# Performance work log

Measured on AMD Instinct MI355X. Metric: run time of the kernel, lower is better.

Reference implementation:

```python
import jax, jax.numpy as jnp
import numpy as np
from jax import lax

DIM = 256
NUM_HEADS = 8
AREA = 4
HEAD_DIM = DIM // NUM_HEADS


def setup_inputs() -> dict:
    key = jax.random.key(0)
    ks = jax.random.split(key, 7)
    B, C, H, W = 4, DIM, 64, 64
    x = jax.random.normal(ks[0], (B, C, H, W), dtype=jnp.float32)
    s = 0.02
    w_qkv = jax.random.normal(ks[1], (3 * C, C), dtype=jnp.float32) * s
    b_qkv = jnp.zeros((3 * C,), dtype=jnp.float32)
    w_pe = jax.random.normal(ks[2], (C, 1, 7, 7), dtype=jnp.float32) * s  # depthwise
    b_pe = jnp.zeros((C,), dtype=jnp.float32)
    w_proj = jax.random.normal(ks[3], (C, C), dtype=jnp.float32) * s
    b_proj = jnp.zeros((C,), dtype=jnp.float32)
    return {"x": x, "w_qkv": w_qkv, "b_qkv": b_qkv, "w_pe": w_pe,
            "b_pe": b_pe, "w_proj": w_proj, "b_proj": b_proj}


def _conv1x1(x, w, b):
    # x: [B,C,H,W], w: [O,C] -> [B,O,H,W]
    return jnp.einsum('bchw,oc->bohw', x, w) + b[None, :, None, None]


def _dwconv7(x, w, b):
    # depthwise 7x7, pad 3, groups = C
    y = lax.conv_general_dilated(
        x, w, window_strides=(1, 1), padding=[(3, 3), (3, 3)],
        dimension_numbers=('NCHW', 'OIHW', 'NCHW'),
        feature_group_count=x.shape[1])
    return y + b[None, :, None, None]


def reference(x, w_qkv, b_qkv, w_pe, b_pe, w_proj, b_proj):
    B, C, H, W = x.shape
    N = H * W
    nh, hd, area = NUM_HEADS, HEAD_DIM, AREA
    Na = N // area
    Ba = B * area

    qkv = _conv1x1(x, w_qkv, b_qkv)                    # [B,3C,H,W]
    qkv = qkv.reshape(B, 3 * C, N).transpose(0, 2, 1)  # [B,N,3C]
    qkv = qkv.reshape(Ba, Na, nh, 3, hd)               # split heads / q,k,v
    q = qkv[:, :, :, 0, :]                             # [Ba,Na,nh,hd]
    k = qkv[:, :, :, 1, :]
    v = qkv[:, :, :, 2, :]

    scale = jnp.asarray(hd, x.dtype) ** -0.5
    attn = jnp.einsum('bihd,bjhd->bhij', q, k) * scale  # [Ba,nh,Na,Na]
    attn = jax.nn.softmax(attn, axis=-1)
    out = jnp.einsum('bhij,bjhd->bihd', attn, v)        # [Ba,Na,nh,hd]

    out = out.reshape(B, N, C)
    v_full = v.reshape(B, N, C)
    out = out.reshape(B, H, W, C).transpose(0, 3, 1, 2)      # [B,C,H,W]
    v_full = v_full.reshape(B, H, W, C).transpose(0, 3, 1, 2)

    out = out + _dwconv7(v_full, w_pe, b_pe)
    return _conv1x1(out, w_proj, b_proj)
```

## Files before the change

kernel.cpp:

```cpp
#include <hip/hip_runtime.h>
#include <hip/hip_bf16.h>


typedef __attribute__((ext_vector_type(8))) short bf16x8;
typedef __attribute__((ext_vector_type(4))) short bf16x4;
typedef __attribute__((ext_vector_type(8))) unsigned short u16x8;
typedef __attribute__((ext_vector_type(4))) float f32x4;
typedef unsigned short u16;

__device__ __forceinline__ short f2bf(float f) {
    unsigned u = __builtin_bit_cast(unsigned, f);
    u = u + 0x7fffu + ((u >> 16) & 1u);
    return (short)(u >> 16);
}
__device__ __forceinline__ float bf2f(u16 u) {
    return __builtin_bit_cast(float, (unsigned)u << 16);
}
__device__ __forceinline__ float fexp2(float x) {
#if __has_builtin(__builtin_amdgcn_exp2f)
    return __builtin_amdgcn_exp2f(x);
#else
    return exp2f(x);
#endif
}
__device__ __forceinline__ unsigned cvt_pk_bf16(float lo, float hi) {
    unsigned r;
    asm("v_cvt_pk_bf16_f32 %0, %1, %2" : "=v"(r) : "v"(lo), "v"(hi));
    return r;
}

__global__ __launch_bounds__(256) void qkv_gemm(const float* __restrict__ X,
                                                const float* __restrict__ W,
                                                const float* __restrict__ bias,
                                                u16* __restrict__ out,
                                                u16* __restrict__ Vt) {
    __shared__ short Alds[64][40];
    __shared__ short Blds[64][40];
    const int t = threadIdx.x;
    const int wv = t >> 6, lane = t & 63;
    const int g = lane >> 4, cc = lane & 15;
    const int wg = blockIdx.x;
    const int hi = wg / 96, rem = wg % 96;
    const int R0 = (hi * 8 + (rem & 7)) * 64;
    const int col0 = (rem >> 3) * 64;
    const int b = R0 >> 12, n0 = R0 & 4095;
    f32x4 acc[4] = {};

    const int a_kk = t >> 4;
    const int a_ii = (t & 15) * 4;
    const int b_col = t >> 2;
    const int b_kp  = (t & 3) * 8;

    for (int k0 = 0; k0 < 256; k0 += 32) {
        __syncthreads();
        #pragma unroll
        for (int it = 0; it < 2; ++it) {
            const int kk = a_kk + it * 16;
            const float4 v = *reinterpret_cast<const float4*>(
                X + (((size_t)(b * 256 + k0 + kk)) << 12) + n0 + a_ii);
            Alds[a_ii + 0][kk] = f2bf(v.x);
            Alds[a_ii + 1][kk] = f2bf(v.y);
            Alds[a_ii + 2][kk] = f2bf(v.z);
            Alds[a_ii + 3][kk] = f2bf(v.w);
        }
        {
            const float* wp = W + (size_t)(col0 + b_col) * 256 + k0 + b_kp;
            const float4 v0 = *reinterpret_cast<const float4*>(wp);
            const float4 v1 = *reinterpret_cast<const float4*>(wp + 4);
            bf16x8 pk;
            pk[0] = f2bf(v0.x); pk[1] = f2bf(v0.y); pk[2] = f2bf(v0.z); pk[3] = f2bf(v0.w);
            pk[4] = f2bf(v1.x); pk[5] = f2bf(v1.y); pk[6] = f2bf(v1.z); pk[7] = f2bf(v1.w);
            *reinterpret_cast<bf16x8*>(&Blds[b_col][b_kp]) = pk;
        }
        __syncthreads();
        const bf16x8 af = *reinterpret_cast<const bf16x8*>(&Alds[wv * 16 + cc][g * 8]);
        #pragma unroll
        for (int nt = 0; nt < 4; ++nt) {
            const bf16x8 bfr = *reinterpret_cast<const bf16x8*>(&Blds[nt * 16 + cc][g * 8]);
            acc[nt] = __builtin_amdgcn_mfma_f32_16x16x32_bf16(af, bfr, acc[nt], 0, 0, 0);
        }
    }
    #pragma unroll
    for (int nt = 0; nt < 4; ++nt) {
        const int col = col0 + nt * 16 + cc;
        const float bv = bias[col];
        const int m96 = col % 96;
        const bool isv = (m96 >= 64);
        const int vc = (col / 96) * 32 + (m96 - 64);
        #pragma unroll
        for (int r = 0; r < 4; ++r) {
            const int row = R0 + wv * 16 + g * 4 + r;
            const u16 val = (u16)f2bf(acc[nt][r] + bv);
            out[(size_t)row * 768 + col] = val;
            if (isv)
                Vt[(((size_t)(b * 256 + vc)) << 12) + (row & 4095)] = val;
        }
    }
}

__global__ __launch_bounds__(256) void attn_kernel(const u16* __restrict__ QKV,
                                                   float* __restrict__ aout) {
    __shared__ u16 Klds[64][32];
    __shared__ u16 Vlds[32][68];
    const int t = threadIdx.x;
    const int wv = t >> 6, lane = t & 63;
    const int g = lane >> 4, cc = lane & 15;
    const int h  = blockIdx.x;
    const int qc = blockIdx.y;
    const int ba = blockIdx.z;
    const float SCALE = 0.17677669529663687f * 1.44269504088896340736f;
    const size_t base = (size_t)ba * 1024 * 768 + h * 96;

    bf16x8 qf[2];
    #pragma unroll
    for (int s = 0; s < 2; ++s) {
        const u16x8 qr = *reinterpret_cast<const u16x8*>(
            QKV + base + (size_t)(qc * 128 + s * 64 + wv * 16 + cc) * 768 + g * 8);
        #pragma unroll
        for (int j = 0; j < 8; ++j) qf[s][j] = f2bf(bf2f(qr[j]) * SCALE);
    }

    f32x4 o[2][2] = {};
    float m[2] = {-3e38f, -3e38f}, l[2] = {0.f, 0.f};

    const int key_s = t >> 2;
    const int dp    = (t & 3) * 8;
    const u16* kgp = QKV + base + 32 + (size_t)key_s * 768 + dp;
    const u16* vgp = kgp + 32;

    u16x8 kpre = *reinterpret_cast<const u16x8*>(kgp);
    u16x8 vpre = *reinterpret_cast<const u16x8*>(vgp);

    for (int kt = 0; kt < 16; ++kt) {
        __syncthreads();
        *reinterpret_cast<u16x8*>(&Klds[key_s][dp]) = kpre;
        #pragma unroll
        for (int i = 0; i < 8; ++i) Vlds[dp + i][key_s] = vpre[i];
        __syncthreads();
        if (kt < 15) {
            kpre = *reinterpret_cast<const u16x8*>(kgp + (size_t)(kt + 1) * 64 * 768);
            vpre = *reinterpret_cast<const u16x8*>(vgp + (size_t)(kt + 1) * 64 * 768);
        }

        bf16x8 kf[4];
        #pragma unroll
        for (int t16 = 0; t16 < 4; ++t16)
            kf[t16] = *reinterpret_cast<const bf16x8*>(&Klds[t16 * 16 + cc][g * 8]);
        bf16x8 va[2][2];
        #pragma unroll
        for (int hh = 0; hh < 2; ++hh)
            #pragma unroll
            for (int kg = 0; kg < 2; ++kg) {
                const bf16x4 lo = *reinterpret_cast<const bf16x4*>(&Vlds[hh * 16 + cc][kg * 32 + 4 * g]);
                const bf16x4 hi = *reinterpret_cast<const bf16x4*>(&Vlds[hh * 16 + cc][kg * 32 + 16 + 4 * g]);
                va[hh][kg] = __builtin_shufflevector(lo, hi, 0, 1, 2, 3, 4, 5, 6, 7);
            }

        #pragma unroll
        for (int s = 0; s < 2; ++s) {
            const f32x4 z = {};
            f32x4 sc[4];
            #pragma unroll
            for (int t16 = 0; t16 < 4; ++t16)
                sc[t16] = __builtin_amdgcn_mfma_f32_16x16x32_bf16(kf[t16], qf[s], z, 0, 0, 0);

            float mt = sc[0][0];
            #pragma unroll
            for (int t16 = 0; t16 < 4; ++t16)
                #pragma unroll
                for (int r = 0; r < 4; ++r) mt = fmaxf(mt, sc[t16][r]);
            mt = fmaxf(mt, __shfl_xor(mt, 16, 64));
            mt = fmaxf(mt, __shfl_xor(mt, 32, 64));
            const float mn = fmaxf(m[s], mt);
            const float fac = fexp2(m[s] - mn);
            m[s] = mn;

            float p[4][4];
            float rs = 0.f;
            #pragma unroll
            for (int t16 = 0; t16 < 4; ++t16)
                #pragma unroll
                for (int r = 0; r < 4; ++r) {
                    p[t16][r] = fexp2(sc[t16][r] - mn);
                    rs += p[t16][r];
                }
            rs += __shfl_xor(rs, 16, 64);
            rs += __shfl_xor(rs, 32, 64);
            l[s] = l[s] * fac + rs;
            o[s][0] *= fac;
            o[s][1] *= fac;

            union PW { int w[4]; bf16x8 v; } pb0, pb1;
            pb0.w[0] = (int)cvt_pk_bf16(p[0][0], p[0][1]);
            pb0.w[1] = (int)cvt_pk_bf16(p[0][2], p[0][3]);
            pb0.w[2] = (int)cvt_pk_bf16(p[1][0], p[1][1]);
            pb0.w[3] = (int)cvt_pk_bf16(p[1][2], p[1][3]);
            pb1.w[0] = (int)cvt_pk_bf16(p[2][0], p[2][1]);
            pb1.w[1] = (int)cvt_pk_bf16(p[2][2], p[2][3]);
            pb1.w[2] = (int)cvt_pk_bf16(p[3][0], p[3][1]);
            pb1.w[3] = (int)cvt_pk_bf16(p[3][2], p[3][3]);

            o[s][0] = __builtin_amdgcn_mfma_f32_16x16x32_bf16(va[0][0], pb0.v, o[s][0], 0, 0, 0);
            o[s][0] = __builtin_amdgcn_mfma_f32_16x16x32_bf16(va[0][1], pb1.v, o[s][0], 0, 0, 0);
            o[s][1] = __builtin_amdgcn_mfma_f32_16x16x32_bf16(va[1][0], pb0.v, o[s][1], 0, 0, 0);
            o[s][1] = __builtin_amdgcn_mfma_f32_16x16x32_bf16(va[1][1], pb1.v, o[s][1], 0, 0, 0);
        }
    }

    #pragma unroll
    for (int s = 0; s < 2; ++s) {
        const float inv = 1.f / l[s];
        const int q = qc * 128 + s * 64 + wv * 16 + cc;
        float* op = aout + (size_t)(ba * 1024 + q) * 256 + h * 32;
        f32x4 st0 = o[s][0] * inv;
        f32x4 st1 = o[s][1] * inv;
        *reinterpret_cast<f32x4*>(op + 4 * g)      = st0;
        *reinterpret_cast<f32x4*>(op + 16 + 4 * g) = st1;
    }
}

__global__ __launch_bounds__(256) void pe_conv(const u16* __restrict__ Vt,
                                               const float* __restrict__ wpe,
                                               const float* __restrict__ bpe,
                                               float* __restrict__ pebuf) {
    __shared__ __align__(16) float P[70][76];
    const int t = threadIdx.x;
    const int bc = blockIdx.x;
    const int c = bc & 255;

    {
        f32x4 z = {};
        f32x4* p4 = reinterpret_cast<f32x4*>(&P[0][0]);
        #pragma unroll
        for (int i = 0; i < 6; ++i) {
            const int idx = t + i * 256;
            if (idx < 1330) p4[idx] = z;
        }
    }
    __syncthreads();
    {
        const int row = t >> 2, xo = (t & 3) * 16;
        const u16* src = Vt + (((size_t)bc) << 12) + row * 64 + xo;
        const u16x8 v0 = *reinterpret_cast<const u16x8*>(src);
        const u16x8 v1 = *reinterpret_cast<const u16x8*>(src + 8);
        #pragma unroll
        for (int j = 0; j < 8; ++j) {
            P[row + 3][xo + 3 + j]  = bf2f(v0[j]);
            P[row + 3][xo + 11 + j] = bf2f(v1[j]);
        }
    }
    float wk[49];
    #pragma unroll
    for (int i = 0; i < 49; ++i) wk[i] = wpe[c * 49 + i];
    const float bias = bpe[c];
    __syncthreads();

    const int y = t >> 2, x0 = (t & 3) * 16;
    float acc[16];
    #pragma unroll
    for (int j = 0; j < 16; ++j) acc[j] = bias;

    #pragma unroll
    for (int dy = 0; dy < 7; ++dy) {
        float win[24];
        #pragma unroll
        for (int w4 = 0; w4 < 6; ++w4)
            *reinterpret_cast<f32x4*>(&win[w4 * 4]) =
                *reinterpret_cast<const f32x4*>(&P[y + dy][x0 + w4 * 4]);
        #pragma unroll
        for (int dx = 0; dx < 7; ++dx) {
            const float wgt = wk[dy * 7 + dx];
            #pragma unroll
            for (int xx = 0; xx < 16; ++xx)
                acc[xx] = fmaf(wgt, win[xx + dx], acc[xx]);
        }
    }

    float* dst = pebuf + (((size_t)bc) << 12) + y * 64 + x0;
    #pragma unroll
    for (int w4 = 0; w4 < 4; ++w4)
        *reinterpret_cast<f32x4*>(dst + w4 * 4) =
            *reinterpret_cast<const f32x4*>(&acc[w4 * 4]);
}

__global__ __launch_bounds__(256) void proj_gemm(const float* __restrict__ A,
                                                 const float* __restrict__ PE,
                                                 const float* __restrict__ W,
                                                 const float* __restrict__ bias,
                                                 float* __restrict__ out) {
    __shared__ union {
        struct { short A[64][40]; short B[64][40]; } s;
        float T[64][65];
    } u;
    const int t = threadIdx.x;
    const int wv = t >> 6, lane = t & 63;
    const int g = lane >> 4, cc = lane & 15;
    const int wg = blockIdx.x;
    const int hi = wg / 32, rem = wg % 32;
    const int R0 = (hi * 8 + (rem & 7)) * 64;
    const int col0 = (rem >> 3) * 64;
    const int b = R0 >> 12, n0 = R0 & 4095;
    const int a_i  = t >> 2;
    const int a_kp = (t & 3) * 8;
    f32x4 acc[4] = {};

    for (int k0 = 0; k0 < 256; k0 += 32) {
        __syncthreads();
        {
            const float* ap = A + (size_t)(R0 + a_i) * 256 + k0 + a_kp;
            const float4 v0 = *reinterpret_cast<const float4*>(ap);
            const float4 v1 = *reinterpret_cast<const float4*>(ap + 4);
            const float* pp = PE + (((size_t)(b * 256 + k0 + a_kp)) << 12) + n0 + a_i;
            bf16x8 pk;
            pk[0] = f2bf(v0.x + pp[0]);
            pk[1] = f2bf(v0.y + pp[(size_t)1 << 12]);
            pk[2] = f2bf(v0.z + pp[(size_t)2 << 12]);
            pk[3] = f2bf(v0.w + pp[(size_t)3 << 12]);
            pk[4] = f2bf(v1.x + pp[(size_t)4 << 12]);
            pk[5] = f2bf(v1.y + pp[(size_t)5 << 12]);
            pk[6] = f2bf(v1.z + pp[(size_t)6 << 12]);
            pk[7] = f2bf(v1.w + pp[(size_t)7 << 12]);
            *reinterpret_cast<bf16x8*>(&u.s.A[a_i][a_kp]) = pk;

            const float* wp = W + (size_t)(col0 + a_i) * 256 + k0 + a_kp;
            const float4 w0 = *reinterpret_cast<const float4*>(wp);
            const float4 w1 = *reinterpret_cast<const float4*>(wp + 4);
            bf16x8 pw;
            pw[0] = f2bf(w0.x); pw[1] = f2bf(w0.y); pw[2] = f2bf(w0.z); pw[3] = f2bf(w0.w);
            pw[4] = f2bf(w1.x); pw[5] = f2bf(w1.y); pw[6] = f2bf(w1.z); pw[7] = f2bf(w1.w);
            *reinterpret_cast<bf16x8*>(&u.s.B[a_i][a_kp]) = pw;
        }
        __syncthreads();
        const bf16x8 af = *reinterpret_cast<const bf16x8*>(&u.s.A[wv * 16 + cc][g * 8]);
        #pragma unroll
        for (int nt = 0; nt < 4; ++nt) {
            const bf16x8 bfr = *reinterpret_cast<const bf16x8*>(&u.s.B[nt * 16 + cc][g * 8]);
            acc[nt] = __builtin_amdgcn_mfma_f32_16x16x32_bf16(af, bfr, acc[nt], 0, 0, 0);
        }
    }
    __syncthreads();
    #pragma unroll
    for (int nt = 0; nt < 4; ++nt) {
        const float bv = bias[col0 + nt * 16 + cc];
        #pragma unroll
        for (int r = 0; r < 4; ++r)
            u.T[nt * 16 + cc][wv * 16 + g * 4 + r] = acc[nt][r] + bv;
    }
    __syncthreads();
    #pragma unroll
    for (int it = 0; it < 16; ++it) {
        const int idx = it * 256 + t;
        const int ccc = idx >> 6, rr = idx & 63;
        out[(((size_t)(b * 256 + col0 + ccc)) << 12) + n0 + rr] = u.T[ccc][rr];
    }
}

extern "C" void kernel_launch(void* const* d_in, const int* in_sizes, int n_in,
                              void* d_out, int out_size, void* d_ws, size_t ws_size,
                              hipStream_t stream) {
    const float* x      = (const float*)d_in[0];
    const float* w_qkv  = (const float*)d_in[1];
    const float* b_qkv  = (const float*)d_in[2];
    const float* w_pe   = (const float*)d_in[3];
    const float* b_pe   = (const float*)d_in[4];
    const float* w_proj = (const float*)d_in[5];
    const float* b_proj = (const float*)d_in[6];
    float* out = (float*)d_out;

    char* ws = (char*)d_ws;
    u16*   qkvbuf = (u16*)ws;
    float* aout   = (float*)(ws + 25165824);
    u16*   vt     = (u16*)(ws + 41943040);
    float* pebuf  = (float*)(ws + 50331648);

    qkv_gemm<<<3072, 256, 0, stream>>>(x, w_qkv, b_qkv, qkvbuf, vt);
    attn_kernel<<<dim3(8, 8, 16), 256, 0, stream>>>(qkvbuf, aout);
    pe_conv<<<1024, 256, 0, stream>>>(vt, w_pe, b_pe, pebuf);
    proj_gemm<<<1024, 256, 0, stream>>>(aout, pebuf, w_proj, b_proj, out);
}
```

Measured before the change: 119.9 us.

## Split attention keys into two halves and merge partial softmax in proj GEMM

```diff
diff --git a/kernel.cpp b/kernel.cpp
--- a/kernel.cpp
+++ b/kernel.cpp
@@ -32,7 +32,7 @@
 __global__ __launch_bounds__(256) void qkv_gemm(const float* __restrict__ X,
                                                 const float* __restrict__ W,
                                                 const float* __restrict__ bias,
-                                                u16* __restrict__ out,
+                                                u16* __restrict__ qkout,
                                                 u16* __restrict__ Vt) {
     __shared__ short Alds[64][40];
     __shared__ short Blds[64][40];
@@ -85,21 +85,28 @@
         const int col = col0 + nt * 16 + cc;
         const float bv = bias[col];
         const int m96 = col % 96;
+        const int head = col / 96;
         const bool isv = (m96 >= 64);
-        const int vc = (col / 96) * 32 + (m96 - 64);
         #pragma unroll
         for (int r = 0; r < 4; ++r) {
             const int row = R0 + wv * 16 + g * 4 + r;
             const u16 val = (u16)f2bf(acc[nt][r] + bv);
-            out[(size_t)row * 768 + col] = val;
             if (isv)
-                Vt[(((size_t)(b * 256 + vc)) << 12) + (row & 4095)] = val;
-        }
-    }
-}
-
-__global__ __launch_bounds__(256) void attn_kernel(const u16* __restrict__ QKV,
-                                                   float* __restrict__ aout) {
+                Vt[(((size_t)(b * 256 + head * 32 + (m96 - 64))) << 12) + (row & 4095)] = val;
+            else
+                qkout[(size_t)row * 512 + head * 64 + m96] = val;
+        }
+    }
+}
+
+__global__ __launch_bounds__(256) void attn_kernel(const u16* __restrict__ QK,
+                                                   const u16* __restrict__ VT,
+                                                   float* __restrict__ O0,
+                                                   float* __restrict__ O1,
+                                                   float* __restrict__ L0,
+                                                   float* __restrict__ M0,
+                                                   float* __restrict__ L1,
+                                                   float* __restrict__ M1) {
     __shared__ u16 Klds[64][32];
     __shared__ u16 Vlds[32][68];
     const int t = threadIdx.x;
@@ -107,15 +114,20 @@
     const int g = lane >> 4, cc = lane & 15;
     const int h  = blockIdx.x;
     const int qc = blockIdx.y;
-    const int ba = blockIdx.z;
+    const int zz = blockIdx.z;
+    const int ba = zz >> 1, half = zz & 1;
+    const int koff = half * 512;
+    float* Oh = half ? O1 : O0;
+    float* Lh = half ? L1 : L0;
+    float* Mh = half ? M1 : M0;
     const float SCALE = 0.17677669529663687f * 1.44269504088896340736f;
-    const size_t base = (size_t)ba * 1024 * 768 + h * 96;
+    const size_t qkbase = (size_t)(ba * 1024) * 512 + h * 64;
 
     bf16x8 qf[2];
     #pragma unroll
     for (int s = 0; s < 2; ++s) {
         const u16x8 qr = *reinterpret_cast<const u16x8*>(
-            QKV + base + (size_t)(qc * 128 + s * 64 + wv * 16 + cc) * 768 + g * 8);
+            QK + qkbase + (size_t)(qc * 128 + s * 64 + wv * 16 + cc) * 512 + g * 8);
         #pragma unroll
         for (int j = 0; j < 8; ++j) qf[s][j] = f2bf(bf2f(qr[j]) * SCALE);
     }
@@ -125,21 +137,24 @@
 
     const int key_s = t >> 2;
     const int dp    = (t & 3) * 8;
-    const u16* kgp = QKV + base + 32 + (size_t)key_s * 768 + dp;
-    const u16* vgp = kgp + 32;
+    const u16* kgp = QK + qkbase + (size_t)(koff + key_s) * 512 + 32 + dp;
+    const int vd  = t >> 3;
+    const int vx8 = (t & 7) * 8;
+    const int b_img = ba >> 2, area = ba & 3;
+    const u16* vgp = VT + (((size_t)(b_img * 256 + h * 32 + vd)) << 12)
+                        + area * 1024 + koff + vx8;
 
     u16x8 kpre = *reinterpret_cast<const u16x8*>(kgp);
     u16x8 vpre = *reinterpret_cast<const u16x8*>(vgp);
 
-    for (int kt = 0; kt < 16; ++kt) {
+    for (int kt = 0; kt < 8; ++kt) {
         __syncthreads();
         *reinterpret_cast<u16x8*>(&Klds[key_s][dp]) = kpre;
-        #pragma unroll
-        for (int i = 0; i < 8; ++i) Vlds[dp + i][key_s] = vpre[i];
-        __syncthreads();
-        if (kt < 15) {
-            kpre = *reinterpret_cast<const u16x8*>(kgp + (size_t)(kt + 1) * 64 * 768);
-            vpre = *reinterpret_cast<const u16x8*>(vgp + (size_t)(kt + 1) * 64 * 768);
+        *reinterpret_cast<u16x8*>(&Vlds[vd][vx8])   = vpre;
+        __syncthreads();
+        if (kt < 7) {
+            kpre = *reinterpret_cast<const u16x8*>(kgp + (size_t)(kt + 1) * 64 * 512);
+            vpre = *reinterpret_cast<const u16x8*>(vgp + (kt + 1) * 64);
         }
 
         bf16x8 kf[4];
@@ -209,13 +224,16 @@
 
     #pragma unroll
     for (int s = 0; s < 2; ++s) {
-        const float inv = 1.f / l[s];
         const int q = qc * 128 + s * 64 + wv * 16 + cc;
-        float* op = aout + (size_t)(ba * 1024 + q) * 256 + h * 32;
-        f32x4 st0 = o[s][0] * inv;
-        f32x4 st1 = o[s][1] * inv;
-        *reinterpret_cast<f32x4*>(op + 4 * g)      = st0;
-        *reinterpret_cast<f32x4*>(op + 16 + 4 * g) = st1;
+        const int row = ba * 1024 + q;
+        float* op = Oh + (size_t)row * 256 + h * 32;
+        *reinterpret_cast<f32x4*>(op + 4 * g)      = o[s][0];
+        *reinterpret_cast<f32x4*>(op + 16 + 4 * g) = o[s][1];
+        if (g == 0) {
+            const int idx = row * 8 + h;
+            Lh[idx] = l[s];
+            Mh[idx] = m[s];
+        }
     }
 }
 
@@ -283,7 +301,12 @@
             *reinterpret_cast<const f32x4*>(&acc[w4 * 4]);
 }
 
-__global__ __launch_bounds__(256) void proj_gemm(const float* __restrict__ A,
+__global__ __launch_bounds__(256) void proj_gemm(const float* __restrict__ O0b,
+                                                 const float* __restrict__ O1b,
+                                                 const float* __restrict__ L0,
+                                                 const float* __restrict__ M0,
+                                                 const float* __restrict__ L1,
+                                                 const float* __restrict__ M1,
                                                  const float* __restrict__ PE,
                                                  const float* __restrict__ W,
                                                  const float* __restrict__ bias,
@@ -307,19 +330,31 @@
     for (int k0 = 0; k0 < 256; k0 += 32) {
         __syncthreads();
         {
-            const float* ap = A + (size_t)(R0 + a_i) * 256 + k0 + a_kp;
-            const float4 v0 = *reinterpret_cast<const float4*>(ap);
-            const float4 v1 = *reinterpret_cast<const float4*>(ap + 4);
+            const int row = R0 + a_i;
+            const int hh8 = (k0 + a_kp) >> 5;
+            const int lmix = row * 8 + hh8;
+            const float M0v = M0[lmix], M1v = M1[lmix];
+            const float mstar = fmaxf(M0v, M1v);
+            const float f0 = fexp2(M0v - mstar);
+            const float f1 = fexp2(M1v - mstar);
+            const float invl = 1.0f / (L0[lmix] * f0 + L1[lmix] * f1);
+            const float c0 = f0 * invl, c1 = f1 * invl;
+            const float* p0 = O0b + (size_t)row * 256 + k0 + a_kp;
+            const float* p1 = O1b + (size_t)row * 256 + k0 + a_kp;
+            const float4 x0lo = *reinterpret_cast<const float4*>(p0);
+            const float4 x0hi = *reinterpret_cast<const float4*>(p0 + 4);
+            const float4 x1lo = *reinterpret_cast<const float4*>(p1);
+            const float4 x1hi = *reinterpret_cast<const float4*>(p1 + 4);
             const float* pp = PE + (((size_t)(b * 256 + k0 + a_kp)) << 12) + n0 + a_i;
             bf16x8 pk;
-            pk[0] = f2bf(v0.x + pp[0]);
-            pk[1] = f2bf(v0.y + pp[(size_t)1 << 12]);
-            pk[2] = f2bf(v0.z + pp[(size_t)2 << 12]);
-            pk[3] = f2bf(v0.w + pp[(size_t)3 << 12]);
-            pk[4] = f2bf(v1.x + pp[(size_t)4 << 12]);
-            pk[5] = f2bf(v1.y + pp[(size_t)5 << 12]);
-            pk[6] = f2bf(v1.z + pp[(size_t)6 << 12]);
-            pk[7] = f2bf(v1.w + pp[(size_t)7 << 12]);
+            pk[0] = f2bf(x0lo.x * c0 + x1lo.x * c1 + pp[0]);
+            pk[1] = f2bf(x0lo.y * c0 + x1lo.y * c1 + pp[(size_t)1 << 12]);
+            pk[2] = f2bf(x0lo.z * c0 + x1lo.z * c1 + pp[(size_t)2 << 12]);
+            pk[3] = f2bf(x0lo.w * c0 + x1lo.w * c1 + pp[(size_t)3 << 12]);
+            pk[4] = f2bf(x0hi.x * c0 + x1hi.x * c1 + pp[(size_t)4 << 12]);
+            pk[5] = f2bf(x0hi.y * c0 + x1hi.y * c1 + pp[(size_t)5 << 12]);
+            pk[6] = f2bf(x0hi.z * c0 + x1hi.z * c1 + pp[(size_t)6 << 12]);
+            pk[7] = f2bf(x0hi.w * c0 + x1hi.w * c1 + pp[(size_t)7 << 12]);
             *reinterpret_cast<bf16x8*>(&u.s.A[a_i][a_kp]) = pk;
 
             const float* wp = W + (size_t)(col0 + a_i) * 256 + k0 + a_kp;
@@ -368,13 +403,19 @@
     float* out = (float*)d_out;
 
     char* ws = (char*)d_ws;
-    u16*   qkvbuf = (u16*)ws;
-    float* aout   = (float*)(ws + 25165824);
-    u16*   vt     = (u16*)(ws + 41943040);
-    float* pebuf  = (float*)(ws + 50331648);
-
-    qkv_gemm<<<3072, 256, 0, stream>>>(x, w_qkv, b_qkv, qkvbuf, vt);
-    attn_kernel<<<dim3(8, 8, 16), 256, 0, stream>>>(qkvbuf, aout);
-    pe_conv<<<1024, 256, 0, stream>>>(vt, w_pe, b_pe, pebuf);
-    proj_gemm<<<1024, 256, 0, stream>>>(aout, pebuf, w_proj, b_proj, out);
-}
+    u16*   qk    = (u16*)ws;
+    float* pe    = (float*)ws;
+    float* o0    = (float*)(ws + 16777216);
+    float* o1    = (float*)(ws + 33554432);
+    u16*   vt    = (u16*)(ws + 50331648);
+    float* l0    = (float*)(ws + 58720256);
+    float* m0    = (float*)(ws + 59244544);
+    float* l1    = (float*)(ws + 59768832);
+    float* m1    = (float*)(ws + 60293120);
+
+    qkv_gemm<<<3072, 256, 0, stream>>>(x, w_qkv, b_qkv, qk, vt);
+    attn_kernel<<<dim3(8, 8, 32), 256, 0, stream>>>(qk, vt, o0, o1, l0, m0, l1, m1);
+    pe_conv<<<1024, 256, 0, stream>>>(vt, w_pe, b_pe, pe);
+    proj_gemm<<<1024, 256, 0, stream>>>(o0, o1, l0, m0, l1, m1, pe,
+                                        w_proj, b_proj, out);
+}
```

Result: no change. 119.4 us (-0.4%).
